# Performance work log

Measured on AMD Instinct MI355X. Metric: run time of the kernel, lower is better.

The kernel has to match this reference:

```python
import jax, jax.numpy as jnp
from jax import lax
import numpy as np

B, L, N_NODES, EMB, TDIM, H, NCLS = 512, 200, 100000, 128, 10, 256, 2
IN = TDIM + EMB  # 138


def setup_inputs() -> dict:
    key = jax.random.key(0)
    ks = jax.random.split(key, 16)
    x = jax.random.randint(ks[0], (B, L, 2), 0, N_NODES, dtype=jnp.int64)
    s = 0.05
    inp = {
        'x': x,
        'emb_table': jax.random.normal(ks[1], (N_NODES, EMB), jnp.float32) * s,
        'ts_W': jnp.ones((1, TDIM), jnp.float32),
        'w_ih_f': jax.random.normal(ks[2], (4 * H, IN), jnp.float32) * s,
        'w_hh_f': jax.random.normal(ks[3], (4 * H, H), jnp.float32) * s,
        'b_ih_f': jax.random.normal(ks[4], (4 * H,), jnp.float32) * s,
        'b_hh_f': jax.random.normal(ks[5], (4 * H,), jnp.float32) * s,
        'w_ih_b': jax.random.normal(ks[6], (4 * H, IN), jnp.float32) * s,
        'w_hh_b': jax.random.normal(ks[7], (4 * H, H), jnp.float32) * s,
        'b_ih_b': jax.random.normal(ks[8], (4 * H,), jnp.float32) * s,
        'b_hh_b': jax.random.normal(ks[9], (4 * H,), jnp.float32) * s,
        'fc_W': jax.random.normal(ks[10], (NCLS, 2 * H), jnp.float32) * s,
        'fc_b': jax.random.normal(ks[11], (NCLS,), jnp.float32) * s,
    }
    return inp


def _lstm_dir(x_seq, w_ih, w_hh, b_ih, b_hh, reverse):
    # x_seq: [B, L, F]; PyTorch gate order i, f, g, o
    bsz = x_seq.shape[0]
    h_dim = w_hh.shape[1]
    xg = jnp.einsum('blf,gf->blg', x_seq, w_ih) + b_ih + b_hh  # [B, L, 4H]
    xs = jnp.swapaxes(xg, 0, 1)  # [L, B, 4H]
    if reverse:
        xs = xs[::-1]

    def step(carry, xg_t):
        h, c = carry
        g = xg_t + h @ w_hh.T
        i, f, gg, o = jnp.split(g, 4, axis=-1)
        c = jax.nn.sigmoid(f) * c + jax.nn.sigmoid(i) * jnp.tanh(gg)
        h = jax.nn.sigmoid(o) * jnp.tanh(c)
        return (h, c), h

    z = jnp.zeros((bsz, h_dim), x_seq.dtype)
    _, hs = lax.scan(step, (z, z), xs)
    hs = jnp.swapaxes(hs, 0, 1)  # [B, L, H]
    if reverse:
        hs = hs[:, ::-1]
    return hs


def reference(x, emb_table, ts_W, w_ih_f, w_hh_f, b_ih_f, b_hh_f,
              w_ih_b, w_hh_b, b_ih_b, b_hh_b, fc_W, fc_b):
    # timestamp embedding: [B, L, 1] @ [1, 10] -> [B, L, 10]
    t = x[:, :, 0:1].astype(jnp.float32)
    t_emb = t @ ts_W
    # F.normalize(p=2, dim=1): L2-normalize over the sequence axis
    norm = jnp.sqrt(jnp.sum(t_emb * t_emb, axis=1, keepdims=True))
    t_emb = t_emb / jnp.maximum(norm, 1e-12)

    # vectorized node-embedding gather; id == -1 -> zero vector
    ids = x[:, :, 1]
    gathered = emb_table[jnp.clip(ids, 0, None)]  # [B, L, 128]
    l_emb = jnp.where((ids >= 0)[..., None], gathered, jnp.zeros((), gathered.dtype))

    embedding = jnp.concatenate([t_emb, l_emb], axis=2)  # [B, L, 138]

    h_f = _lstm_dir(embedding, w_ih_f, w_hh_f, b_ih_f, b_hh_f, reverse=False)
    h_b = _lstm_dir(embedding, w_ih_b, w_hh_b, b_ih_b, b_hh_b, reverse=True)
    out = jnp.concatenate([h_f, h_b], axis=-1)  # [B, L, 2H]

    return out[:, -1, :] @ fc_W.T + fc_b  # [B, num_classes]
```

## Files before the change

### kernel.cpp

```cpp
#include <hip/hip_runtime.h>
#include <stdint.h>


typedef unsigned short u16;
typedef __bf16 bf16x8 __attribute__((ext_vector_type(8)));
typedef float  f32x4  __attribute__((ext_vector_type(4)));
typedef float  f32x2  __attribute__((ext_vector_type(2)));
typedef int    i32x4v __attribute__((ext_vector_type(4)));
typedef int    i32x8v __attribute__((ext_vector_type(8)));

#define B_    512
#define L_    200
#define EMB_  128
#define TDIM_ 10
#define IN_   138
#define INP_  160
#define H_    256
#define G4_   1024
#define T_    200
#define DS_   (1.0f/1024.0f)
#define LOG2E 1.4426950408889634f
#define EXP2(x) __builtin_amdgcn_exp2f(x)
#define RCP(x)  __builtin_amdgcn_rcpf(x)

static __device__ __forceinline__ float bf2f(u16 u) {
  union { uint32_t i; float f; } v; v.i = ((uint32_t)u) << 16; return v.f;
}
static __device__ __forceinline__ u16 f2bf(float f) {
  __bf16 h = (__bf16)f; return __builtin_bit_cast(u16, h);
}
static __device__ __forceinline__ float bflo(uint32_t u) {
  return __builtin_bit_cast(float, (uint32_t)(u << 16));
}
static __device__ __forceinline__ float bfhi(uint32_t u) {
  return __builtin_bit_cast(float, (uint32_t)(u & 0xffff0000u));
}
static __device__ __forceinline__ float sigf(float x) {
  return RCP(1.0f + EXP2(-x * LOG2E));
}
static __device__ __forceinline__ float tanh_(float x) {
  x = fminf(fmaxf(x, -15.f), 15.f);
  float e = EXP2(2.0f * LOG2E * x);
  return (e - 1.0f) * RCP(e + 1.0f);
}
static __device__ __forceinline__ f32x4 mfma16(bf16x8 a, bf16x8 b, f32x4 c) {
  return __builtin_amdgcn_mfma_f32_16x16x32_bf16(a, b, c, 0, 0, 0);
}
static __device__ __forceinline__ f32x4 vzero4() {
  f32x4 v; v[0] = 0.f; v[1] = 0.f; v[2] = 0.f; v[3] = 0.f; return v;
}

__global__ void k_prep_mx(const float* __restrict__ whh, int* __restrict__ wf8) {
  int idx = blockIdx.x * blockDim.x + threadIdx.x;
  int d = idx & 7;
  int lane = (idx >> 3) & 63;
  int fs = idx >> 9;
  int kp2 = fs & 1, tt = (fs >> 1) & 7, w = fs >> 4;
  int mm = lane & 15, q = lane >> 4;
  int g = (w + 8 * tt) * 16 + mm;
  int k = kp2 * 128 + q * 32 + d * 4;
  const float* src = whh + g * 256 + k;
  int v = __builtin_amdgcn_cvt_pk_fp8_f32(src[0] * 64.f, src[1] * 64.f, 0, false);
  v     = __builtin_amdgcn_cvt_pk_fp8_f32(src[2] * 64.f, src[3] * 64.f, v, true);
  wf8[idx] = v;
}

__global__ __launch_bounds__(256) void k_feat(
    const int* __restrict__ x, const float* __restrict__ emb,
    const float* __restrict__ tsW, u16* __restrict__ feat) {
  __shared__ float sh_t[224];
  __shared__ int   sh_id[224];
  __shared__ float sh_s[4];
  const int b = blockIdx.x, tid = threadIdx.x;
  float v = 0.f;
  if (tid < L_) {
    int2 p = *(const int2*)&x[(b * L_ + tid) * 2];
    float t = (float)p.x;
    sh_t[tid] = t;
    sh_id[tid] = p.y;
    v = t * t;
  }
  #pragma unroll
  for (int o = 32; o; o >>= 1) v += __shfl_down(v, o);
  if ((tid & 63) == 0) sh_s[tid >> 6] = v;
  __syncthreads();
  const float sq = sqrtf(sh_s[0] + sh_s[1] + sh_s[2] + sh_s[3]);
  for (int i = tid; i < L_ * INP_; i += 256) {
    int l = i / INP_, c = i - l * INP_;
    float v2 = 0.f;
    if (c < TDIM_) {
      float wd = tsW[c];
      float den = fmaxf(fabsf(wd) * sq, 1e-12f);
      v2 = sh_t[l] * wd * RCP(den);
    } else if (c < IN_) {
      int id = sh_id[l];
      float e = emb[(long)(id < 0 ? 0 : id) * EMB_ + (c - TDIM_)];
      v2 = (id >= 0) ? e : 0.f;
    }
    feat[(long)b * (L_ * INP_) + i] = f2bf(v2);
  }
}

__global__ __launch_bounds__(512, 2) void k_xg(
    const u16* __restrict__ feat, const float* __restrict__ wih,
    const float* __restrict__ bih, const float* __restrict__ bhh,
    u16* __restrict__ xg) {
  __shared__ u16 Bs[256 * 176];
  const int nt = blockIdx.x;
  const int mt = blockIdx.y;
  const int tid = threadIdx.x;
  const int w = tid >> 6, lane = tid & 63;
  const int q = lane >> 4, nm = lane & 15;
  for (int i2 = tid; i2 < 256 * 88; i2 += 512) {
    int gl = i2 / 88, f2 = (i2 % 88) * 2;
    int pk = 0;
    if (f2 < IN_) {
      float2 v = *(const float2*)(wih + (long)(nt * 256 + gl) * IN_ + f2);
      pk = (int)f2bf(v.x) | ((int)f2bf(v.y) << 16);
    }
    *(int*)&Bs[gl * 176 + f2] = pk;
  }
  float bias[16];
  #pragma unroll
  for (int nu = 0; nu < 16; ++nu) {
    int g = nt * 256 + nu * 16 + nm;
    bias[nu] = bih[g] + bhh[g];
  }
  __syncthreads();
  f32x4 acc[2][16];
  #pragma unroll
  for (int m = 0; m < 2; ++m)
    #pragma unroll
    for (int nu = 0; nu < 16; ++nu) acc[m][nu] = vzero4();
  const u16* arow = feat + (long)(mt * 256 + w * 32) * INP_;
  #pragma unroll
  for (int kp = 0; kp < 5; ++kp) {
    bf16x8 a0 = *(const bf16x8*)(arow + (nm * INP_ + kp * 32 + q * 8));
    bf16x8 a1 = *(const bf16x8*)(arow + ((16 + nm) * INP_ + kp * 32 + q * 8));
    #pragma unroll
    for (int nu = 0; nu < 16; ++nu) {
      bf16x8 bb = *(const bf16x8*)&Bs[(nu * 16 + nm) * 176 + kp * 32 + q * 8];
      acc[0][nu] = mfma16(a0, bb, acc[0][nu]);
      acc[1][nu] = mfma16(a1, bb, acc[1][nu]);
    }
  }
  u16* Os = Bs;
  #pragma unroll
  for (int p = 0; p < 2; ++p) {
    __syncthreads();
    if ((w >> 2) == p) {
      #pragma unroll
      for (int nu = 0; nu < 16; ++nu)
        #pragma unroll
        for (int m = 0; m < 2; ++m)
          #pragma unroll
          for (int r = 0; r < 4; ++r) {
            int row = (w & 3) * 32 + m * 16 + 4 * q + r;
            Os[row * 264 + nu * 16 + nm] = f2bf((acc[m][nu][r] + bias[nu]) * 1024.f);
          }
    }
    __syncthreads();
    #pragma unroll
    for (int it = 0; it < 8; ++it) {
      int flat = it * 512 + tid;
      int row = flat >> 5, c = flat & 31;
      uint4 v = *(const uint4*)&Os[row * 264 + c * 8];
      *(uint4*)&xg[(long)(mt * 256 + p * 128 + row) * G4_ + nt * 256 + c * 8] = v;
    }
  }
}

#define F8MA(accv, Aa, Bv) \
  asm volatile("v_mfma_f32_16x16x128_f8f6f4 %0, %1, %2, %0" \
               : "+v"(accv) : "a"(Aa), "v"(Bv));
#define F8MV(accv, Av, Bv) \
  asm volatile("v_mfma_f32_16x16x128_f8f6f4 %0, %1, %2, %0" \
               : "+v"(accv) : "v"(Av), "v"(Bv));
#define AINIT(i) \
  f32x4 acc##i; acc##i[0] = bflo(pf##i.x); acc##i[1] = bfhi(pf##i.x); \
  acc##i[2] = bflo(pf##i.y); acc##i[3] = bfhi(pf##i.y);
#define PFL(i, ptr) pf##i = *(const uint2*)((ptr) + (16 * (w + 16 * (i)) + 4 * q));
#define EPIPAIR(P, cs2, hv2) f32x2 hv2; { \
  f32x2 ai = {acc0[2*(P)], acc0[2*(P)+1]}; \
  f32x2 af = {acc1[2*(P)], acc1[2*(P)+1]}; \
  f32x2 ag = {acc2[2*(P)], acc2[2*(P)+1]}; \
  f32x2 ao = {acc3[2*(P)], acc3[2*(P)+1]}; \
  f32x2 xi = ai * c_sig, xf = af * c_sig, xo = ao * c_sig, xgv = ag * c_tg; \
  f32x2 ei, ef, eo, eg, ec; \
  ei[0] = EXP2(xi[0]); ei[1] = EXP2(xi[1]); \
  ef[0] = EXP2(xf[0]); ef[1] = EXP2(xf[1]); \
  eo[0] = EXP2(xo[0]); eo[1] = EXP2(xo[1]); \
  eg[0] = EXP2(xgv[0]); eg[1] = EXP2(xgv[1]); \
  f32x2 t1 = ef + 1.f; \
  f32x2 r1; r1[0] = RCP(t1[0]); r1[1] = RCP(t1[1]); \
  f32x2 t2 = (ei + 1.f) * (eg + 1.f); \
  f32x2 r2; r2[0] = RCP(t2[0]); r2[1] = RCP(t2[1]); \
  f32x2 c = cs2 * r1 + (eg - 1.f) * r2; \
  cs2 = c; \
  f32x2 xc = c * c_tc; \
  ec[0] = EXP2(xc[0]); ec[1] = EXP2(xc[1]); \
  f32x2 t3 = (eo + 1.f) * (ec + 1.f); \
  f32x2 r3; r3[0] = RCP(t3[0]); r3[1] = RCP(t3[1]); \
  hv2 = (ec * 16.f - 16.f) * r3; }

#define FSOLD(M, kp2) (((M) & 7) * 16 + ((M) >> 3) * 2 + (kp2))
#define WLOAD(M, kp2) (*(const i32x8v*)(wf8 + ((long)(FSOLD(M, kp2)) * 64 + lane) * 8))

__global__ __launch_bounds__(1024, 4) void k_lstm_f(
    const int* __restrict__ wf8, const u16* __restrict__ xg,
    float* __restrict__ hf,
    const u16* __restrict__ feat, const float* __restrict__ wihb,
    const float* __restrict__ bihb, const float* __restrict__ bhhb,
    float* __restrict__ hb) {
  __shared__ i32x8v ldsW[32 * 64];
  __shared__ int hls[2][16 * 68];

  if (blockIdx.x >= 32) {
    const int b0 = (blockIdx.x - 32) * 8;
    const int tid = threadIdx.x;
    float* fv = (float*)hls;
    for (int i = tid; i < 8 * IN_; i += 1024) {
      int r = i / IN_, c = i - r * IN_;
      fv[r * IN_ + c] = bf2f(feat[((long)(b0 + r) * L_ + (L_ - 1)) * INP_ + c]);
    }
    __syncthreads();
    const int col = tid & 255, rq = tid >> 8;
    float gi0 = bihb[col] + bhhb[col];
    float gg0 = bihb[512 + col] + bhhb[512 + col];
    float go0 = bihb[768 + col] + bhhb[768 + col];
    float gi1 = gi0, gg1 = gg0, go1 = go0;
    const float* wi_ = wihb + (long)col * IN_;
    const float* wg_ = wihb + (long)(512 + col) * IN_;
    const float* wo_ = wihb + (long)(768 + col) * IN_;
    const float* f0 = fv + (rq * 2) * IN_;
    const float* f1 = fv + (rq * 2 + 1) * IN_;
    for (int f = 0; f < IN_; ++f) {
      float a = wi_[f], g = wg_[f], o = wo_[f];
      float x0 = f0[f], x1 = f1[f];
      gi0 += a * x0; gi1 += a * x1;
      gg0 += g * x0; gg1 += g * x1;
      go0 += o * x0; go1 += o * x1;
    }
    float c0 = sigf(gi0) * tanh_(gg0);
    float c1 = sigf(gi1) * tanh_(gg1);
    hb[(long)(b0 + rq * 2) * H_ + col]     = sigf(go0) * tanh_(c0);
    hb[(long)(b0 + rq * 2 + 1) * H_ + col] = sigf(go1) * tanh_(c1);
    return;
  }

  const int tid = threadIdx.x;
  const int w = tid >> 6;
  const int lane = tid & 63;
  const int q = lane >> 4;
  const int nn = lane & 15;
  const int b = blockIdx.x * 16 + nn;
  const float c_sig = -DS_ * LOG2E;
  const float c_tg  = 2.f * DS_ * LOG2E;
  const float c_tc  = 2.f * LOG2E;

  i32x8v A00 = WLOAD(w, 0),      A01 = WLOAD(w, 1);
  i32x8v A10 = WLOAD(w + 16, 0), A11 = WLOAD(w + 16, 1);
  i32x8v A20 = WLOAD(w + 32, 0), A21 = WLOAD(w + 32, 1);
  ldsW[(w * 2 + 0) * 64 + lane] = WLOAD(w + 48, 0);
  ldsW[(w * 2 + 1) * 64 + lane] = WLOAD(w + 48, 1);
  for (int i = tid; i < 16 * 68; i += 1024) hls[0][i] = 0;

  const u16* xgb = xg + (long)b * (L_ * G4_);
  uint2 pf0, pf1, pf2, pf3;
  PFL(0, xgb) PFL(1, xgb) PFL(2, xgb) PFL(3, xgb)
  f32x2 cs0; cs0[0] = 0.f; cs0[1] = 0.f;
  f32x2 cs1; cs1[0] = 0.f; cs1[1] = 0.f;
  __syncthreads();

  #pragma unroll 1
  for (int t = 0; t < T_; ++t) {
    const int* hr = hls[t & 1];
    i32x8v B0 = *(const i32x8v*)&hr[nn * 68 + q * 8];
    i32x8v B1 = *(const i32x8v*)&hr[nn * 68 + 32 + q * 8];
    i32x8v L0 = ldsW[(w * 2 + 0) * 64 + lane];
    i32x8v L1 = ldsW[(w * 2 + 1) * 64 + lane];
    AINIT(0) AINIT(1) AINIT(2) AINIT(3)
    {
      const u16* xn = xgb + (long)(t + 1 < T_ ? t + 1 : t) * G4_;
      PFL(0, xn) PFL(1, xn) PFL(2, xn) PFL(3, xn)
    }
    F8MA(acc0, A00, B0) F8MA(acc1, A10, B0) F8MA(acc2, A20, B0) F8MV(acc3, L0, B0)
    F8MA(acc0, A01, B1) F8MA(acc1, A11, B1) F8MA(acc2, A21, B1) F8MV(acc3, L1, B1)
    asm volatile("s_nop 7\n\ts_nop 7"
                 : "+v"(acc0), "+v"(acc1), "+v"(acc2), "+v"(acc3));
    int* hw = hls[1 - (t & 1)];
    EPIPAIR(0, cs0, hv0)
    EPIPAIR(1, cs1, hv1)
    int pk = __builtin_amdgcn_cvt_pk_fp8_f32(hv0[0], hv0[1], 0, false);
    pk     = __builtin_amdgcn_cvt_pk_fp8_f32(hv1[0], hv1[1], pk, true);
    hw[nn * 68 + 4 * w + q] = pk;
    if (t == T_ - 1) {
      f32x4 ov;
      ov[0] = hv0[0] * 0.0625f; ov[1] = hv0[1] * 0.0625f;
      ov[2] = hv1[0] * 0.0625f; ov[3] = hv1[1] * 0.0625f;
      *(f32x4*)&hf[(long)b * H_ + 16 * w + 4 * q] = ov;
    }
    __asm__ volatile("" ::: "memory");
    __builtin_amdgcn_s_waitcnt(0xc07f);
    __builtin_amdgcn_s_barrier();
    __asm__ volatile("" ::: "memory");
  }
}

__global__ void k_fc(const float* __restrict__ hf, const float* __restrict__ hb,
                     const float* __restrict__ fcw, const float* __restrict__ fcb,
                     float* __restrict__ out) {
  int b = blockIdx.x;
  int lane = threadIdx.x;
  float p0 = 0.f, p1 = 0.f;
  #pragma unroll
  for (int k = lane; k < 2 * H_; k += 64) {
    float v = (k < H_) ? hf[b * H_ + k] : hb[b * H_ + (k - H_)];
    p0 += v * fcw[k];
    p1 += v * fcw[2 * H_ + k];
  }
  #pragma unroll
  for (int o = 32; o; o >>= 1) {
    p0 += __shfl_down(p0, o);
    p1 += __shfl_down(p1, o);
  }
  if (lane == 0) {
    out[b * 2 + 0] = p0 + fcb[0];
    out[b * 2 + 1] = p1 + fcb[1];
  }
}

extern "C" void kernel_launch(void* const* d_in, const int* in_sizes, int n_in,
                              void* d_out, int out_size, void* d_ws, size_t ws_size,
                              hipStream_t stream) {
  const int*   x    = (const int*)  d_in[0];
  const float* emb  = (const float*)d_in[1];
  const float* tsW  = (const float*)d_in[2];
  const float* wihf = (const float*)d_in[3];
  const float* whhf = (const float*)d_in[4];
  const float* bihf = (const float*)d_in[5];
  const float* bhhf = (const float*)d_in[6];
  const float* wihb = (const float*)d_in[7];
  const float* bihb = (const float*)d_in[9];
  const float* bhhb = (const float*)d_in[10];
  const float* fcw  = (const float*)d_in[11];
  const float* fcb  = (const float*)d_in[12];
  float* out = (float*)d_out;

  char* ws = (char*)d_ws;
  int*   wf8  = (int*)  (ws + 2048);
  u16*   feat = (u16*)  (ws + 264192);
  u16*   xg   = (u16*)  (ws + 33032192);
  float* hf   = (float*)(ws + 242747392);
  float* hb   = (float*)(ws + 243271680);

  k_prep_mx<<<dim3(256),    dim3(256),  0, stream>>>(whhf, wf8);
  k_feat   <<<dim3(512),    dim3(256),  0, stream>>>(x, emb, tsW, feat);
  k_xg     <<<dim3(4, 400), dim3(512),  0, stream>>>(feat, wihf, bihf, bhhf, xg);
  k_lstm_f <<<dim3(96),     dim3(1024), 0, stream>>>(wf8, xg, hf,
                                                     feat, wihb, bihb, bhhb, hb);
  k_fc     <<<dim3(512),    dim3(64),   0, stream>>>(hf, hb, fcw, fcb, out);
}
```

Measured before the change: 727.9 us.

## Split LSTM batch across twice the blocks and halve the per-lane epilogue work

The forward LSTM kernel now gives each block 8 batch rows instead of 16 and launches 64 recurrent blocks instead of 32. Inside the 16-column MFMA, each batch column is duplicated, so the two lanes holding the same batch each take half of the gate outputs through the sigmoid/tanh epilogue. The goal is to shorten the serial per-step epilogue on the critical path of the 200-step recurrence and spread the work over more CUs. In exchange, half of each MFMA's columns are redundant and twice as many blocks each re-load the recurrent weights.

```diff
diff --git a/kernel.cpp b/kernel.cpp
--- a/kernel.cpp
+++ b/kernel.cpp
@@ -180,12 +180,8 @@
   f32x4 acc##i; acc##i[0] = bflo(pf##i.x); acc##i[1] = bfhi(pf##i.x); \
   acc##i[2] = bflo(pf##i.y); acc##i[3] = bfhi(pf##i.y);
 #define PFL(i, ptr) pf##i = *(const uint2*)((ptr) + (16 * (w + 16 * (i)) + 4 * q));
-#define EPIPAIR(P, cs2, hv2) f32x2 hv2; { \
-  f32x2 ai = {acc0[2*(P)], acc0[2*(P)+1]}; \
-  f32x2 af = {acc1[2*(P)], acc1[2*(P)+1]}; \
-  f32x2 ag = {acc2[2*(P)], acc2[2*(P)+1]}; \
-  f32x2 ao = {acc3[2*(P)], acc3[2*(P)+1]}; \
-  f32x2 xi = ai * c_sig, xf = af * c_sig, xo = ao * c_sig, xgv = ag * c_tg; \
+#define EPI(ai, af, ag, ao, cs2, hv2) f32x2 hv2; { \
+  f32x2 xi = (ai) * c_sig, xf = (af) * c_sig, xo = (ao) * c_sig, xgv = (ag) * c_tg; \
   f32x2 ei, ef, eo, eg, ec; \
   ei[0] = EXP2(xi[0]); ei[1] = EXP2(xi[1]); \
   ef[0] = EXP2(xf[0]); ef[1] = EXP2(xf[1]); \
@@ -215,8 +211,8 @@
   __shared__ i32x8v ldsW[32 * 64];
   __shared__ int hls[2][16 * 68];
 
-  if (blockIdx.x >= 32) {
-    const int b0 = (blockIdx.x - 32) * 8;
+  if (blockIdx.x >= 64) {
+    const int b0 = (blockIdx.x - 64) * 8;
     const int tid = threadIdx.x;
     float* fv = (float*)hls;
     for (int i = tid; i < 8 * IN_; i += 1024) {
@@ -253,7 +249,9 @@
   const int lane = tid & 63;
   const int q = lane >> 4;
   const int nn = lane & 15;
-  const int b = blockIdx.x * 16 + nn;
+  const int sl = nn & 7;
+  const int hi = (nn >> 3) & 1;
+  const int b = blockIdx.x * 8 + sl;
   const float c_sig = -DS_ * LOG2E;
   const float c_tg  = 2.f * DS_ * LOG2E;
   const float c_tc  = 2.f * LOG2E;
@@ -268,15 +266,14 @@
   const u16* xgb = xg + (long)b * (L_ * G4_);
   uint2 pf0, pf1, pf2, pf3;
   PFL(0, xgb) PFL(1, xgb) PFL(2, xgb) PFL(3, xgb)
-  f32x2 cs0; cs0[0] = 0.f; cs0[1] = 0.f;
-  f32x2 cs1; cs1[0] = 0.f; cs1[1] = 0.f;
+  f32x2 cs; cs[0] = 0.f; cs[1] = 0.f;
   __syncthreads();
 
   #pragma unroll 1
   for (int t = 0; t < T_; ++t) {
     const int* hr = hls[t & 1];
-    i32x8v B0 = *(const i32x8v*)&hr[nn * 68 + q * 8];
-    i32x8v B1 = *(const i32x8v*)&hr[nn * 68 + 32 + q * 8];
+    i32x8v B0 = *(const i32x8v*)&hr[sl * 68 + q * 8];
+    i32x8v B1 = *(const i32x8v*)&hr[sl * 68 + 32 + q * 8];
     i32x8v L0 = ldsW[(w * 2 + 0) * 64 + lane];
     i32x8v L1 = ldsW[(w * 2 + 1) * 64 + lane];
     AINIT(0) AINIT(1) AINIT(2) AINIT(3)
@@ -289,16 +286,16 @@
     asm volatile("s_nop 7\n\ts_nop 7"
                  : "+v"(acc0), "+v"(acc1), "+v"(acc2), "+v"(acc3));
     int* hw = hls[1 - (t & 1)];
-    EPIPAIR(0, cs0, hv0)
-    EPIPAIR(1, cs1, hv1)
-    int pk = __builtin_amdgcn_cvt_pk_fp8_f32(hv0[0], hv0[1], 0, false);
-    pk     = __builtin_amdgcn_cvt_pk_fp8_f32(hv1[0], hv1[1], pk, true);
-    hw[nn * 68 + 4 * w + q] = pk;
+    f32x2 ai; ai[0] = hi ? acc0[2] : acc0[0]; ai[1] = hi ? acc0[3] : acc0[1];
+    f32x2 af; af[0] = hi ? acc1[2] : acc1[0]; af[1] = hi ? acc1[3] : acc1[1];
+    f32x2 ag; ag[0] = hi ? acc2[2] : acc2[0]; ag[1] = hi ? acc2[3] : acc2[1];
+    f32x2 ao; ao[0] = hi ? acc3[2] : acc3[0]; ao[1] = hi ? acc3[3] : acc3[1];
+    EPI(ai, af, ag, ao, cs, hv)
+    int pk = __builtin_amdgcn_cvt_pk_fp8_f32(hv[0], hv[1], 0, false);
+    ((unsigned short*)hw)[sl * 136 + 8 * w + 2 * q + hi] = (unsigned short)pk;
     if (t == T_ - 1) {
-      f32x4 ov;
-      ov[0] = hv0[0] * 0.0625f; ov[1] = hv0[1] * 0.0625f;
-      ov[2] = hv1[0] * 0.0625f; ov[3] = hv1[1] * 0.0625f;
-      *(f32x4*)&hf[(long)b * H_ + 16 * w + 4 * q] = ov;
+      f32x2 ov; ov[0] = hv[0] * 0.0625f; ov[1] = hv[1] * 0.0625f;
+      *(f32x2*)&hf[(long)b * H_ + 16 * w + 4 * q + 2 * hi] = ov;
     }
     __asm__ volatile("" ::: "memory");
     __builtin_amdgcn_s_waitcnt(0xc07f);
@@ -357,7 +354,7 @@
   k_prep_mx<<<dim3(256),    dim3(256),  0, stream>>>(whhf, wf8);
   k_feat   <<<dim3(512),    dim3(256),  0, stream>>>(x, emb, tsW, feat);
   k_xg     <<<dim3(4, 400), dim3(512),  0, stream>>>(feat, wihf, bihf, bhhf, xg);
-  k_lstm_f <<<dim3(96),     dim3(1024), 0, stream>>>(wf8, xg, hf,
+  k_lstm_f <<<dim3(128),    dim3(1024), 0, stream>>>(wf8, xg, hf,
                                                      feat, wihb, bihb, bhhb, hb);
   k_fc     <<<dim3(512),    dim3(64),   0, stream>>>(hf, hb, fcw, fcb, out);
 }
```

Result: no change. 727.1 us (-0.1%).
